# Kernel optimization log

Hardware: AMD Instinct MI355X
Metric: run time of the kernel (lower is better)

The kernel has to match this reference:

```python
import jax, jax.numpy as jnp
import numpy as np

B, S, E = 4, 2048, 1024


def setup_inputs() -> dict:
    key = jax.random.key(0)
    ks = jax.random.split(key, 7)
    s = 1.0 / np.sqrt(E)  # torch Linear default init scale (uniform bound)
    inp = {
        "input": jax.random.normal(ks[0], (B, S, E), dtype=jnp.float32),
        "masked": 1,
        "W_q": jax.random.uniform(ks[1], (E, E), jnp.float32, -s, s),
        "b_q": jax.random.uniform(ks[2], (E,), jnp.float32, -s, s),
        "W_k": jax.random.uniform(ks[3], (E, E), jnp.float32, -s, s),
        "b_k": jax.random.uniform(ks[4], (E,), jnp.float32, -s, s),
        "W_v": jax.random.uniform(ks[5], (E, E), jnp.float32, -s, s),
        "b_v": jax.random.uniform(ks[6], (E,), jnp.float32, -s, s),
    }
    return inp


def reference(input, masked, W_q, b_q, W_k, b_k, W_v, b_v):
    # torch.nn.Linear: y = x @ W.T + b
    q = jnp.einsum("bse,fe->bsf", input, W_q) + b_q
    k = jnp.einsum("bse,fe->bsf", input, W_k) + b_k
    v = jnp.einsum("bse,fe->bsf", input, W_v) + b_v
    d = q.shape[-1]
    scores = jnp.einsum("bqd,bkd->bqk", q, k) / jnp.sqrt(jnp.float32(d))
    if masked:
        Sq = scores.shape[1]
        causal = jnp.tril(jnp.ones((Sq, Sq), dtype=bool))  # [S,S], broadcast over batch
        scores = jnp.where(causal, scores, -jnp.inf)
    attn = jax.nn.softmax(scores, axis=-1)
    return jnp.einsum("bqk,bkd->bqd", attn, v)
```

## Files before the change

### kernel.cpp

```cpp
#include <hip/hip_runtime.h>

typedef _Float16 f16;
typedef f16 f16x8 __attribute__((ext_vector_type(8)));
typedef f16 f16x4v __attribute__((ext_vector_type(4)));
typedef f16 f16x2v __attribute__((ext_vector_type(2)));
typedef float f32x4 __attribute__((ext_vector_type(4)));

__device__ __forceinline__ void async_ld16(const void* g, void* l) {
    __builtin_amdgcn_global_load_lds(
        (const __attribute__((address_space(1))) unsigned int*)g,
        (__attribute__((address_space(3))) unsigned int*)l, 16, 0, 0);
}

#define VMC(n) asm volatile("s_waitcnt vmcnt(" #n ")" ::: "memory")
#define BAR __builtin_amdgcn_s_barrier()


#define SSTG_A(b, kh, tOff) do {                                                \
    char* d_ = (char*)smem + (b) * 32768 + (kh) * 8192 + stgBase;               \
    async_ld16(pA  + (tOff) * 64 + (kh) * 32, d_);                              \
    async_ld16(pA1 + (tOff) * 64 + (kh) * 32, d_ + 4096);                       \
} while (0)
#define SSTG_B(b, kh, tOff) do {                                                \
    char* d_ = (char*)smem + (b) * 32768 + 16384 + (kh) * 8192 + stgBase;       \
    async_ld16(pB  + (tOff) * 64 + (kh) * 32, d_);                              \
    async_ld16(pB1 + (tOff) * 64 + (kh) * 32, d_ + 4096);                       \
} while (0)
#define SRD(b, kk) do {                                                         \
    const char* sa_ = (const char*)smem + (b) * 32768 + (kk) * 8192 + aOff;     \
    _Pragma("unroll") for (int m_ = 0; m_ < 4; ++m_)                            \
        af[m_] = *(const f16x8*)(sa_ + m_ * 1024);                              \
    const char* sb_ = (const char*)smem + (b) * 32768 + 16384 + (kk) * 8192 + bOff; \
    _Pragma("unroll") for (int n_ = 0; n_ < 4; ++n_)                            \
        bf[n_] = *(const f16x8*)(sb_ + n_ * 1024);                              \
} while (0)
#define SFENCE do {                                                             \
    asm volatile("s_waitcnt lgkmcnt(0)" ::: "memory");                          \
    __builtin_amdgcn_sched_barrier(0);                                          \
    __builtin_amdgcn_s_setprio(1);                                              \
    _Pragma("unroll") for (int m_ = 0; m_ < 4; ++m_)                            \
        _Pragma("unroll") for (int n_ = 0; n_ < 4; ++n_)                        \
            acc[m_][n_] = __builtin_amdgcn_mfma_f32_16x16x32_f16(af[m_], bf[n_], acc[m_][n_], 0, 0, 0); \
    __builtin_amdgcn_s_setprio(0);                                              \
} while (0)

__global__ __launch_bounds__(256, 2) void scores128(
    const f16* __restrict__ Q, const f16* __restrict__ K,
    f16* __restrict__ P, const int* __restrict__ maskedp)
{
    const int masked = *maskedp;
    const int bx = blockIdx.x, by = blockIdx.y, bz = blockIdx.z;
    if (masked && bx > by) return;
    const int mBase = by * 128, nBase = bx * 128;
    const bool diag = (masked != 0) && (bx == by);

    __shared__ __align__(16) f16 smem[32768];
    const int tid = threadIdx.x;
    const int wave = tid >> 6, lane = tid & 63;
    const int wrow = wave >> 1, wcol = wave & 1;
    const int quad = lane >> 4, l16 = lane & 15;
    const int rowLane = tid >> 2;
    const int cOff = ((tid & 3) ^ ((tid >> 3) & 3)) * 8;
    const int stgBase = wave * 1024;
    const int swz  = (quad ^ ((l16 >> 1) & 3)) * 16;
    const int aOff = (wrow * 64 + l16) * 64 + swz;
    const int bOff = (wcol * 64 + l16) * 64 + swz;

    const f16* Ab = Q + (long)bz * (2048L * 1024);
    const f16* Bb = K + (long)bz * (2048L * 1024);
    const f16* pA  = Ab + (long)(mBase + rowLane) * 1024 + cOff;
    const f16* pA1 = pA + 64 * 1024;
    const f16* pB  = Bb + (long)(nBase + rowLane) * 1024 + cOff;
    const f16* pB1 = pB + 64 * 1024;

    f32x4 acc[4][4];
#pragma unroll
    for (int m = 0; m < 4; ++m)
#pragma unroll
        for (int n = 0; n < 4; ++n) acc[m][n] = (f32x4){0.f, 0.f, 0.f, 0.f};
    f16x8 af[4], bf[4];

    SSTG_A(0, 0, 0); SSTG_B(0, 0, 0);
    SSTG_A(0, 1, 0); SSTG_B(0, 1, 0);
    SSTG_A(1, 0, 1); SSTG_B(1, 0, 1);
    VMC(4);
    BAR;

#pragma unroll 1
    for (int i = 0; i < 7; ++i) {
        SRD(0, 0); SSTG_A(1, 1, 1); SSTG_B(1, 1, 1);
        SFENCE; VMC(8); BAR;
        SRD(0, 1); SSTG_A(0, 0, 2); SSTG_B(0, 0, 2);
        SFENCE; VMC(8); BAR;
        SRD(1, 0); SSTG_A(0, 1, 2); SSTG_B(0, 1, 2);
        SFENCE; VMC(8); BAR;
        SRD(1, 1); SSTG_A(1, 0, 3); SSTG_B(1, 0, 3);
        SFENCE; VMC(8); BAR;
        pA += 128; pA1 += 128; pB += 128; pB1 += 128;
    }
    SRD(0, 0); SSTG_A(1, 1, 1); SSTG_B(1, 1, 1);
    SFENCE; VMC(8); BAR;
    SRD(0, 1);
    SFENCE; VMC(4); BAR;
    SRD(1, 0);
    SFENCE; VMC(0); BAR;
    SRD(1, 1);
    SFENCE;

    f16* Crow = P + (long)bz * (2048L * 2048);
#pragma unroll
    for (int m = 0; m < 4; ++m)
#pragma unroll
        for (int n = 0; n < 4; ++n)
#pragma unroll
            for (int r = 0; r < 4; ++r) {
                const int row = mBase + wrow * 64 + m * 16 + quad * 4 + r;
                const int col = nBase + wcol * 64 + n * 16 + l16;
                float e = __expf(acc[m][n][r] * 0.03125f);
                if (diag && col > row) e = 0.f;
                Crow[(long)row * 2048 + col] = (f16)e;
            }
}

#undef SSTG_A
#undef SSTG_B
#undef SRD
#undef SFENCE

#define QSTG(j, o) do {                                                         \
    char* da_ = (char*)smem + (j) * 24576 + wave * 1024;                        \
    async_ld16(pA0 + (o) * 32, da_);                                            \
    async_ld16(pA1 + (o) * 32, da_ + 4096);                                     \
    char* db_ = (char*)smem + (j) * 24576 + 8192 + wave * 1024;                 \
    async_ld16(pB0 + (o) * 32, db_);                                            \
    async_ld16(pB1 + (o) * 32, db_ + 4096);                                     \
    async_ld16(pB2 + (o) * 32, db_ + 8192);                                     \
    async_ld16(pB3 + (o) * 32, db_ + 12288);                                    \
} while (0)
#define QRD(j) do {                                                             \
    const char* sa_ = (const char*)smem + (j) * 24576 + aOff;                   \
    _Pragma("unroll") for (int m_ = 0; m_ < 8; ++m_)                            \
        af[m_] = *(const f16x8*)(sa_ + m_ * 1024);                              \
    const char* sb_ = (const char*)smem + (j) * 24576 + 8192 + bOff;            \
    _Pragma("unroll") for (int n_ = 0; n_ < 4; ++n_)                            \
        bf[n_] = *(const f16x8*)(sb_ + n_ * 1024);                              \
} while (0)
#define QFENCE do {                                                             \
    asm volatile("s_waitcnt lgkmcnt(0)" ::: "memory");                          \
    __builtin_amdgcn_sched_barrier(0);                                          \
    __builtin_amdgcn_s_setprio(1);                                              \
    _Pragma("unroll") for (int m_ = 0; m_ < 8; ++m_)                            \
        _Pragma("unroll") for (int n_ = 0; n_ < 4; ++n_)                        \
            acc[m_][n_] = __builtin_amdgcn_mfma_f32_16x16x32_f16(af[m_], bf[n_], acc[m_][n_], 0, 0, 0); \
    __builtin_amdgcn_s_setprio(0);                                              \
} while (0)
#define QT(j, j2, o2) do { QRD(j); QSTG(j2, o2); QFENCE; VMC(6); BAR; } while (0)

__global__ __launch_bounds__(256, 2) void qkv128(
    const f16* __restrict__ A, const f16* __restrict__ Bt,
    const float* __restrict__ b_q, const float* __restrict__ b_k,
    const float* __restrict__ b_v,
    f16* __restrict__ Q16, f16* __restrict__ K16, f16* __restrict__ Vt16)
{
    const int orig = blockIdx.x;
    const int xcd = orig & 7;
    const int s = orig >> 3;
    const int by = xcd * 8 + (s & 7);
    const int bx = s >> 3;
    const int mBase = by * 128, nBase = bx * 256;

    __shared__ __align__(16) f16 smem[36864];
    const int tid = threadIdx.x;
    const int wave = tid >> 6, lane = tid & 63;
    const int quad = lane >> 4, l16 = lane & 15;
    const int rowLane = tid >> 2;
    const int cOff = ((tid & 3) ^ ((tid >> 3) & 3)) * 8;
    const int swz  = (quad ^ ((l16 >> 1) & 3)) * 16;
    const int aOff = l16 * 64 + swz;
    const int bOff = (wave * 64 + l16) * 64 + swz;

    const f16* pA0 = A  + (long)(mBase + rowLane) * 1024 + cOff;
    const f16* pA1 = pA0 + 64 * 1024;
    const f16* pB0 = Bt + (long)(nBase + rowLane) * 1024 + cOff;
    const f16* pB1 = pB0 + 64 * 1024;
    const f16* pB2 = pB0 + 128 * 1024;
    const f16* pB3 = pB0 + 192 * 1024;

    f32x4 acc[8][4];
#pragma unroll
    for (int m = 0; m < 8; ++m)
#pragma unroll
        for (int n = 0; n < 4; ++n) acc[m][n] = (f32x4){0.f, 0.f, 0.f, 0.f};
    f16x8 af[8], bf[4];

    QSTG(0, 0); QSTG(1, 1);
    VMC(6);
    BAR;

#pragma unroll 1
    for (int g = 0; g < 10; ++g) {
        QT(0, 2, 2);
        QT(1, 0, 3);
        QT(2, 1, 4);
        pA0 += 96; pA1 += 96; pB0 += 96; pB1 += 96; pB2 += 96; pB3 += 96;
    }
    QRD(0); QFENCE; VMC(0); BAR;
    QRD(1); QFENCE;
    BAR;

    const int seg = nBase >> 10;
    const float* bs = (seg == 0) ? b_q : (seg == 1) ? b_k : b_v;
    const int lcb = (nBase & 1023) + wave * 64;
    float bvv[4];
#pragma unroll
    for (int n = 0; n < 4; ++n) bvv[n] = bs[lcb + n * 16 + l16];

    if (seg < 2) {
        f16* dst = (seg == 0) ? Q16 : K16;
#pragma unroll
        for (int m = 0; m < 8; ++m)
#pragma unroll
            for (int n = 0; n < 4; ++n)
#pragma unroll
                for (int r = 0; r < 4; ++r) {
                    const int row = mBase + m * 16 + quad * 4 + r;
                    dst[(long)row * 1024 + lcb + n * 16 + l16] =
                        (f16)(acc[m][n][r] + bvv[n]);
                }
    } else {
        const int b = mBase >> 11;
        const int s0 = mBase & 2047;
        const int e0 = (nBase & 1023) + wave * 64;
        f16* epiW = smem + wave * (64 * 136);
#pragma unroll
        for (int m = 0; m < 8; ++m)
#pragma unroll
            for (int n = 0; n < 4; ++n) {
                f16x4v pk;
#pragma unroll
                for (int r = 0; r < 4; ++r)
                    pk[r] = (f16)(acc[m][n][r] + bvv[n]);
                *(f16x4v*)&epiW[(n * 16 + l16) * 136 + m * 16 + quad * 4] = pk;
            }
        asm volatile("s_waitcnt lgkmcnt(0)" ::: "memory");
#pragma unroll
        for (int it = 0; it < 16; ++it) {
            const int e = it * 4 + (lane >> 4);
            const f16x8 v = *(const f16x8*)&epiW[e * 136 + (lane & 15) * 8];
            *(f16x8*)(Vt16 + ((long)b * 1024 + e0 + e) * 2048 + s0 +
                      (lane & 15) * 8) = v;
        }
    }
}

#undef QSTG
#undef QRD
#undef QFENCE
#undef QT

#if defined(__has_builtin)
#if __has_builtin(__builtin_amdgcn_fdot2)
#define HAVE_FDOT2 1
#endif
#endif

#ifdef HAVE_FDOT2
#define PSUM do {                                                               \
    const f16x2v one_ = {(f16)1, (f16)1};                                       \
    _Pragma("unroll") for (int m_ = 0; m_ < 4; ++m_) {                          \
        const f16x2v* ph_ = (const f16x2v*)&af[m_];                             \
        _Pragma("unroll") for (int j_ = 0; j_ < 4; ++j_)                        \
            rs[m_] = __builtin_amdgcn_fdot2(ph_[j_], one_, rs[m_], false);      \
    }                                                                           \
} while (0)
#else
#define PSUM do {                                                               \
    _Pragma("unroll") for (int m_ = 0; m_ < 4; ++m_)                            \
        _Pragma("unroll") for (int j_ = 0; j_ < 8; ++j_)                        \
            rs[m_] += (float)af[m_][j_];                                        \
} while (0)
#endif

#define PSTG_A(b, kh, tOff) do {                                                \
    char* d_ = (char*)smem + (b) * 32768 + (kh) * 8192 + stgBase;               \
    async_ld16(pA  + (tOff) * 64 + (kh) * 32, d_);                              \
    async_ld16(pA1 + (tOff) * 64 + (kh) * 32, d_ + 4096);                       \
} while (0)
#define PSTG_B(b, kh, tOff) do {                                                \
    char* d_ = (char*)smem + (b) * 32768 + 16384 + (kh) * 8192 + stgBase;       \
    async_ld16(pB  + (tOff) * 64 + (kh) * 32, d_);                              \
    async_ld16(pB1 + (tOff) * 64 + (kh) * 32, d_ + 4096);                       \
} while (0)
#define PRD(b, kk) do {                                                         \
    const char* sa_ = (const char*)smem + (b) * 32768 + (kk) * 8192 + aOff;     \
    _Pragma("unroll") for (int m_ = 0; m_ < 4; ++m_)                            \
        af[m_] = *(const f16x8*)(sa_ + m_ * 1024);                              \
    const char* sb_ = (const char*)smem + (b) * 32768 + 16384 + (kk) * 8192 + bOff; \
    _Pragma("unroll") for (int n_ = 0; n_ < 4; ++n_)                            \
        bf[n_] = *(const f16x8*)(sb_ + n_ * 1024);                              \
} while (0)
#define PFENCE do {                                                             \
    asm volatile("s_waitcnt lgkmcnt(0)" ::: "memory");                          \
    __builtin_amdgcn_sched_barrier(0);                                          \
    __builtin_amdgcn_s_setprio(1);                                              \
    _Pragma("unroll") for (int m_ = 0; m_ < 4; ++m_)                            \
        _Pragma("unroll") for (int n_ = 0; n_ < 4; ++n_)                        \
            acc[m_][n_] = __builtin_amdgcn_mfma_f32_16x16x32_f16(af[m_], bf[n_], acc[m_][n_], 0, 0, 0); \
    __builtin_amdgcn_s_setprio(0);                                              \
    PSUM;                                                                       \
} while (0)

__global__ __launch_bounds__(256, 2) void pv128(
    const f16* __restrict__ P, const f16* __restrict__ Vt,
    float* __restrict__ out, const int* __restrict__ maskedp)
{
    const int masked = *maskedp;
    const int bx = blockIdx.x, bz = blockIdx.z;
    const int by = (bz >= 2) ? blockIdx.y : (gridDim.y - 1 - blockIdx.y);
    const int mBase = by * 128, nBase = bx * 128;
    const int nIter = masked ? (by + 1) : 16;

    __shared__ __align__(16) f16 smem[32768];
    const int tid = threadIdx.x;
    const int wave = tid >> 6, lane = tid & 63;
    const int wrow = wave >> 1, wcol = wave & 1;
    const int quad = lane >> 4, l16 = lane & 15;
    const int rowLane = tid >> 2;
    const int cOff = ((tid & 3) ^ ((tid >> 3) & 3)) * 8;
    const int stgBase = wave * 1024;
    const int swz  = (quad ^ ((l16 >> 1) & 3)) * 16;
    const int aOff = (wrow * 64 + l16) * 64 + swz;
    const int bOff = (wcol * 64 + l16) * 64 + swz;

    const f16* Pb = P  + (long)bz * (2048L * 2048);
    const f16* Vb = Vt + (long)bz * (1024L * 2048);
    const f16* pA  = Pb + (long)(mBase + rowLane) * 2048 + cOff;
    const f16* pA1 = pA + 64 * 2048;
    const f16* pB  = Vb + (long)(nBase + rowLane) * 2048 + cOff;
    const f16* pB1 = pB + 64 * 2048;

    f32x4 acc[4][4];
#pragma unroll
    for (int m = 0; m < 4; ++m)
#pragma unroll
        for (int n = 0; n < 4; ++n) acc[m][n] = (f32x4){0.f, 0.f, 0.f, 0.f};
    f16x8 af[4], bf[4];
    float rs[4] = {0.f, 0.f, 0.f, 0.f};

    PSTG_A(0, 0, 0); PSTG_B(0, 0, 0);
    PSTG_A(0, 1, 0); PSTG_B(0, 1, 0);
    PSTG_A(1, 0, 1); PSTG_B(1, 0, 1);
    VMC(4);
    BAR;

#pragma unroll 1
    for (int i = 0; i < nIter - 1; ++i) {
        PRD(0, 0); PSTG_A(1, 1, 1); PSTG_B(1, 1, 1);
        PFENCE; VMC(8); BAR;
        PRD(0, 1); PSTG_A(0, 0, 2); PSTG_B(0, 0, 2);
        PFENCE; VMC(8); BAR;
        PRD(1, 0); PSTG_A(0, 1, 2); PSTG_B(0, 1, 2);
        PFENCE; VMC(8); BAR;
        PRD(1, 1); PSTG_A(1, 0, 3); PSTG_B(1, 0, 3);
        PFENCE; VMC(8); BAR;
        pA += 128; pA1 += 128; pB += 128; pB1 += 128;
    }
    PRD(0, 0); PSTG_A(1, 1, 1); PSTG_B(1, 1, 1);
    PFENCE; VMC(8); BAR;
    PRD(0, 1);
    PFENCE; VMC(4); BAR;
    PRD(1, 0);
    PFENCE; VMC(0); BAR;
    PRD(1, 1);
    PFENCE;

#pragma unroll
    for (int m = 0; m < 4; ++m) {
        rs[m] += __shfl_xor(rs[m], 16);
        rs[m] += __shfl_xor(rs[m], 32);
    }

    float* ob = out + (long)bz * (2048L * 1024);
#pragma unroll
    for (int m = 0; m < 4; ++m)
#pragma unroll
        for (int r = 0; r < 4; ++r) {
            const int row = mBase + wrow * 64 + m * 16 + quad * 4 + r;
            const float inv = 1.f / __shfl(rs[m], quad * 4 + r);
#pragma unroll
            for (int n = 0; n < 4; ++n) {
                const int col = nBase + wcol * 64 + n * 16 + l16;
                ob[(long)row * 1024 + col] = acc[m][n][r] * inv;
            }
        }
}

#undef PSTG_A
#undef PSTG_B
#undef PRD
#undef PFENCE
#undef PSUM
#undef VMC
#undef BAR

__global__ void cvt_all(const float* __restrict__ inp,
                        const float* __restrict__ W0,
                        const float* __restrict__ W1,
                        const float* __restrict__ W2,
                        f16* __restrict__ inp16, f16* __restrict__ W3)
{
    const int bxx = blockIdx.x;
    const float* src;
    f16* dst;
    int i;
    if (bxx < 8192) {
        src = inp; dst = inp16;
        i = bxx * 256 + threadIdx.x;
    } else {
        const int wb = bxx - 8192;
        const int which = wb >> 10;
        src = (which == 0) ? W0 : (which == 1) ? W1 : W2;
        dst = W3 + (long)which * 1024 * 1024;
        i = (wb & 1023) * 256 + threadIdx.x;
    }
    const float4 v = ((const float4*)src)[i];
    f16x4v o;
    o[0] = (f16)v.x; o[1] = (f16)v.y; o[2] = (f16)v.z; o[3] = (f16)v.w;
    ((f16x4v*)dst)[i] = o;
}

extern "C" void kernel_launch(void* const* d_in, const int* in_sizes, int n_in,
                              void* d_out, int out_size, void* d_ws, size_t ws_size,
                              hipStream_t stream)
{
    const float* inp = (const float*)d_in[0];
    const int* masked = (const int*)d_in[1];
    const float* Wq = (const float*)d_in[2];
    const float* bq = (const float*)d_in[3];
    const float* Wk = (const float*)d_in[4];
    const float* bk = (const float*)d_in[5];
    const float* Wv = (const float*)d_in[6];
    const float* bv = (const float*)d_in[7];
    float* out = (float*)d_out;

    const int S = 2048, E = 1024;
    const long nTok = (long)4 * S;

    char* ws = (char*)d_ws;
    f16* inp16 = (f16*)ws;   ws += nTok * E * 2;
    f16* W3    = (f16*)ws;   ws += (long)3 * E * E * 2;
    f16* Q16   = (f16*)ws;   ws += nTok * E * 2;
    f16* K16   = (f16*)ws;   ws += nTok * E * 2;
    f16* Vt16  = (f16*)ws;   ws += nTok * E * 2;
    f16* P16   = (f16*)ws;   ws += (long)4 * S * S * 2;

    cvt_all<<<dim3(8192 + 3072), dim3(256), 0, stream>>>(
        inp, Wq, Wk, Wv, inp16, W3);

    qkv128<<<dim3(768), dim3(256), 0, stream>>>(
        inp16, W3, bq, bk, bv, Q16, K16, Vt16);

    scores128<<<dim3(16, 16, 4), dim3(256), 0, stream>>>(
        Q16, K16, P16, masked);

    pv128<<<dim3(8, 16, 4), dim3(256), 0, stream>>>(
        P16, Vt16, out, masked);
}
```

Before: 221.3 us.

## Restructure scores kernel to 2 waves with 128x64 per-wave tiles and 3-stage pipeline

The QK^T scores kernel now runs with 128 threads (2 waves) instead of 256, and each wave computes a 128x64 output strip (8x4 MFMA tiles) rather than 64x64. The K loop is reorganised into a 3-buffer ring of 32-wide K chunks in 48KB of LDS, replacing the previous 2-buffer scheme with split K halves. The aim is more register-level reuse of A fragments per LDS read and fewer barriers per unit of work. In exchange it doubles the accumulator registers per wave, and occupancy depends on the new launch bounds of (128,3).

```diff
diff --git a/kernel.cpp b/kernel.cpp
--- a/kernel.cpp
+++ b/kernel.cpp
@@ -16,21 +16,23 @@
 #define BAR __builtin_amdgcn_s_barrier()
 
 
-#define SSTG_A(b, kh, tOff) do {                                                \
-    char* d_ = (char*)smem + (b) * 32768 + (kh) * 8192 + stgBase;               \
-    async_ld16(pA  + (tOff) * 64 + (kh) * 32, d_);                              \
-    async_ld16(pA1 + (tOff) * 64 + (kh) * 32, d_ + 4096);                       \
-} while (0)
-#define SSTG_B(b, kh, tOff) do {                                                \
-    char* d_ = (char*)smem + (b) * 32768 + 16384 + (kh) * 8192 + stgBase;       \
-    async_ld16(pB  + (tOff) * 64 + (kh) * 32, d_);                              \
-    async_ld16(pB1 + (tOff) * 64 + (kh) * 32, d_ + 4096);                       \
-} while (0)
-#define SRD(b, kk) do {                                                         \
-    const char* sa_ = (const char*)smem + (b) * 32768 + (kk) * 8192 + aOff;     \
-    _Pragma("unroll") for (int m_ = 0; m_ < 4; ++m_)                            \
+#define SSTG(j, o) do {                                                         \
+    char* dA_ = (char*)smem + (j) * 16384 + wave * 1024;                        \
+    async_ld16(pA0 + (o) * 32, dA_);                                            \
+    async_ld16(pA1 + (o) * 32, dA_ + 2048);                                     \
+    async_ld16(pA2 + (o) * 32, dA_ + 4096);                                     \
+    async_ld16(pA3 + (o) * 32, dA_ + 6144);                                     \
+    char* dB_ = (char*)smem + (j) * 16384 + 8192 + wave * 1024;                 \
+    async_ld16(pB0 + (o) * 32, dB_);                                            \
+    async_ld16(pB1 + (o) * 32, dB_ + 2048);                                     \
+    async_ld16(pB2 + (o) * 32, dB_ + 4096);                                     \
+    async_ld16(pB3 + (o) * 32, dB_ + 6144);                                     \
+} while (0)
+#define SRD(j) do {                                                             \
+    const char* sa_ = (const char*)smem + (j) * 16384 + aOff;                   \
+    _Pragma("unroll") for (int m_ = 0; m_ < 8; ++m_)                            \
         af[m_] = *(const f16x8*)(sa_ + m_ * 1024);                              \
-    const char* sb_ = (const char*)smem + (b) * 32768 + 16384 + (kk) * 8192 + bOff; \
+    const char* sb_ = (const char*)smem + (j) * 16384 + 8192 + bOff;            \
     _Pragma("unroll") for (int n_ = 0; n_ < 4; ++n_)                            \
         bf[n_] = *(const f16x8*)(sb_ + n_ * 1024);                              \
 } while (0)
@@ -38,13 +40,14 @@
     asm volatile("s_waitcnt lgkmcnt(0)" ::: "memory");                          \
     __builtin_amdgcn_sched_barrier(0);                                          \
     __builtin_amdgcn_s_setprio(1);                                              \
-    _Pragma("unroll") for (int m_ = 0; m_ < 4; ++m_)                            \
+    _Pragma("unroll") for (int m_ = 0; m_ < 8; ++m_)                            \
         _Pragma("unroll") for (int n_ = 0; n_ < 4; ++n_)                        \
             acc[m_][n_] = __builtin_amdgcn_mfma_f32_16x16x32_f16(af[m_], bf[n_], acc[m_][n_], 0, 0, 0); \
     __builtin_amdgcn_s_setprio(0);                                              \
 } while (0)
-
-__global__ __launch_bounds__(256, 2) void scores128(
+#define ST(j, j2, o2) do { SRD(j); SSTG(j2, o2); SFENCE; VMC(8); BAR; } while (0)
+
+__global__ __launch_bounds__(128, 3) void scores128(
     const f16* __restrict__ Q, const f16* __restrict__ K,
     f16* __restrict__ P, const int* __restrict__ maskedp)
 {
@@ -54,78 +57,68 @@
     const int mBase = by * 128, nBase = bx * 128;
     const bool diag = (masked != 0) && (bx == by);
 
-    __shared__ __align__(16) f16 smem[32768];
+    __shared__ __align__(16) f16 smem[24576];
     const int tid = threadIdx.x;
     const int wave = tid >> 6, lane = tid & 63;
-    const int wrow = wave >> 1, wcol = wave & 1;
     const int quad = lane >> 4, l16 = lane & 15;
     const int rowLane = tid >> 2;
     const int cOff = ((tid & 3) ^ ((tid >> 3) & 3)) * 8;
-    const int stgBase = wave * 1024;
     const int swz  = (quad ^ ((l16 >> 1) & 3)) * 16;
-    const int aOff = (wrow * 64 + l16) * 64 + swz;
-    const int bOff = (wcol * 64 + l16) * 64 + swz;
+    const int aOff = l16 * 64 + swz;
+    const int bOff = (wave * 64 + l16) * 64 + swz;
 
     const f16* Ab = Q + (long)bz * (2048L * 1024);
     const f16* Bb = K + (long)bz * (2048L * 1024);
-    const f16* pA  = Ab + (long)(mBase + rowLane) * 1024 + cOff;
-    const f16* pA1 = pA + 64 * 1024;
-    const f16* pB  = Bb + (long)(nBase + rowLane) * 1024 + cOff;
-    const f16* pB1 = pB + 64 * 1024;
-
-    f32x4 acc[4][4];
-#pragma unroll
-    for (int m = 0; m < 4; ++m)
+    const f16* pA0 = Ab + (long)(mBase + rowLane) * 1024 + cOff;
+    const f16* pA1 = pA0 + 32 * 1024;
+    const f16* pA2 = pA0 + 64 * 1024;
+    const f16* pA3 = pA0 + 96 * 1024;
+    const f16* pB0 = Bb + (long)(nBase + rowLane) * 1024 + cOff;
+    const f16* pB1 = pB0 + 32 * 1024;
+    const f16* pB2 = pB0 + 64 * 1024;
+    const f16* pB3 = pB0 + 96 * 1024;
+
+    f32x4 acc[8][4];
+#pragma unroll
+    for (int m = 0; m < 8; ++m)
 #pragma unroll
         for (int n = 0; n < 4; ++n) acc[m][n] = (f32x4){0.f, 0.f, 0.f, 0.f};
-    f16x8 af[4], bf[4];
-
-    SSTG_A(0, 0, 0); SSTG_B(0, 0, 0);
-    SSTG_A(0, 1, 0); SSTG_B(0, 1, 0);
-    SSTG_A(1, 0, 1); SSTG_B(1, 0, 1);
-    VMC(4);
+    f16x8 af[8], bf[4];
+
+    SSTG(0, 0); SSTG(1, 1);
+    VMC(8);
     BAR;
 
 #pragma unroll 1
-    for (int i = 0; i < 7; ++i) {
-        SRD(0, 0); SSTG_A(1, 1, 1); SSTG_B(1, 1, 1);
-        SFENCE; VMC(8); BAR;
-        SRD(0, 1); SSTG_A(0, 0, 2); SSTG_B(0, 0, 2);
-        SFENCE; VMC(8); BAR;
-        SRD(1, 0); SSTG_A(0, 1, 2); SSTG_B(0, 1, 2);
-        SFENCE; VMC(8); BAR;
-        SRD(1, 1); SSTG_A(1, 0, 3); SSTG_B(1, 0, 3);
-        SFENCE; VMC(8); BAR;
-        pA += 128; pA1 += 128; pB += 128; pB1 += 128;
-    }
-    SRD(0, 0); SSTG_A(1, 1, 1); SSTG_B(1, 1, 1);
-    SFENCE; VMC(8); BAR;
-    SRD(0, 1);
-    SFENCE; VMC(4); BAR;
-    SRD(1, 0);
-    SFENCE; VMC(0); BAR;
-    SRD(1, 1);
-    SFENCE;
+    for (int g = 0; g < 10; ++g) {
+        ST(0, 2, 2);
+        ST(1, 0, 3);
+        ST(2, 1, 4);
+        pA0 += 96; pA1 += 96; pA2 += 96; pA3 += 96;
+        pB0 += 96; pB1 += 96; pB2 += 96; pB3 += 96;
+    }
+    SRD(0); SFENCE; VMC(0); BAR;
+    SRD(1); SFENCE;
 
     f16* Crow = P + (long)bz * (2048L * 2048);
 #pragma unroll
-    for (int m = 0; m < 4; ++m)
+    for (int m = 0; m < 8; ++m)
 #pragma unroll
         for (int n = 0; n < 4; ++n)
 #pragma unroll
             for (int r = 0; r < 4; ++r) {
-                const int row = mBase + wrow * 64 + m * 16 + quad * 4 + r;
-                const int col = nBase + wcol * 64 + n * 16 + l16;
+                const int row = mBase + m * 16 + quad * 4 + r;
+                const int col = nBase + wave * 64 + n * 16 + l16;
                 float e = __expf(acc[m][n][r] * 0.03125f);
                 if (diag && col > row) e = 0.f;
                 Crow[(long)row * 2048 + col] = (f16)e;
             }
 }
 
-#undef SSTG_A
-#undef SSTG_B
+#undef SSTG
 #undef SRD
 #undef SFENCE
+#undef ST
 
 #define QSTG(j, o) do {                                                         \
     char* da_ = (char*)smem + (j) * 24576 + wave * 1024;                        \
@@ -460,7 +453,7 @@
     qkv128<<<dim3(768), dim3(256), 0, stream>>>(
         inp16, W3, bq, bk, bv, Q16, K16, Vt16);
 
-    scores128<<<dim3(16, 16, 4), dim3(256), 0, stream>>>(
+    scores128<<<dim3(16, 16, 4), dim3(128), 0, stream>>>(
         Q16, K16, P16, masked);
 
     pv128<<<dim3(8, 16, 4), dim3(256), 0, stream>>>(
```

Measured after the change: 232.8 us. 5.2% more time.
